# Optimization experiments

Measured on AMD Instinct MI355X. Metric: run time of the kernel, lower is better.

## Reference

```python
import jax, jax.numpy as jnp
import numpy as np

K = 5  # box-blur width along disparity axis

def _blur_disparity(x):
    # depthwise conv1d with ones(K)/K kernel, zero 'same' padding, along axis 1
    N, D, H, W = x.shape
    xp = jnp.pad(x, ((0, 0), (K // 2, K // 2), (0, 0), (0, 0)))
    acc = xp[:, 0:D]
    for s in range(1, K):
        acc = acc + xp[:, s:s + D]
    return acc / K

def _modal_mask(x):
    N, D, H, W = x.shape
    index = jnp.argmax(x, axis=1, keepdims=True)                 # [N,1,H,W] int
    d = jnp.arange(D, dtype=x.dtype).reshape(1, D, 1, 1)
    d2 = jnp.arange(D + 1, dtype=x.dtype).reshape(1, D + 1, 1, 1)
    ones = jnp.ones((N, 1, H, W), dtype=x.dtype)
    x_diff_r = jnp.diff(x, axis=1, prepend=ones, append=ones)    # [N,D+1,H,W]
    x_diff_l = jnp.diff(x, axis=1, prepend=ones)                 # [N,D,H,W]
    # right edge of dominant mode: first positive diff strictly right of peak
    ind_r = ((x_diff_r * (d2 > index)) > 0).astype(jnp.int32)
    index_r = jnp.argmax(ind_r, axis=1, keepdims=True) - 1
    # left edge: last negative diff at/left of peak
    ind_l = ((x_diff_l * (d <= index)) < 0).astype(jnp.int32)
    index_l = D - 1 - jnp.argmax(jnp.flip(ind_l, axis=1), axis=1, keepdims=True)
    mask1 = (d >= index_l) & (d <= index_r)
    r = jnp.minimum(index_r - index, index - index_l)
    mask2 = (d >= index - r) & (d <= index + r)
    valid = jnp.abs(2 * index - index_r - index_l) < 3           # near-symmetric mode
    return jnp.where(valid, mask1, mask2)                        # bool [N,D,H,W]

def setup_inputs() -> dict:
    key = jax.random.key(0)
    N, D, H, W = 2, 192, 256, 512
    x = jax.random.uniform(key, (N, D, H, W), dtype=jnp.float32)
    return {"x": x}

def reference(x) -> jnp.ndarray:
    N, D, H, W = x.shape
    disp = jnp.arange(D, dtype=x.dtype).reshape(1, D, 1, 1)
    x_blur = _blur_disparity(x)
    mask = _modal_mask(x_blur)
    y = x * mask                       # primary mode mass
    z = x - y
    x_blur2 = x_blur * (~mask)
    z = z * _modal_mask(x_blur2)       # secondary mode mass
    valid = (jnp.sum(y, axis=1) >= jnp.sum(z, axis=1)).astype(jnp.float32)[:, None]
    xm = valid * y + (1.0 - valid) * z
    xm = xm / jnp.sum(xm, axis=1, keepdims=True)
    out = jnp.sum(xm * disp, axis=1, keepdims=True)  # [N,1,H,W]
    return out
```

## Files before the change

kernel.cpp:

```cpp
#include <hip/hip_runtime.h>
#include <math.h>

namespace {
constexpr int D     = 192;
constexpr int HW    = 256 * 512;
constexpr int TOTAL = 2 * HW;

__device__ __forceinline__ float div5(float s) {
    const float c = 0.2f;
    float q = s * c;
    float r = __builtin_fmaf(-5.0f, q, s);
    return __builtin_fmaf(r, c, q);
}

__device__ __forceinline__ bool in_range(int d, int lo, unsigned width) {
    return (unsigned)(d - lo) <= width;
}

struct Machine {
    float bprev, maxv;
    int   index, last_fall, index_l, index_r;
    bool  r_found;

    __device__ __forceinline__ void init() {
        bprev = 1.0f;
        maxv  = -INFINITY;
        index = 0; last_fall = 0; index_l = 0;
        index_r = D - 1;
        r_found = false;
    }

    __device__ __forceinline__ void step(int d, float b) {
        float diff = b - bprev;
        bool fall  = diff < 0.0f;
        last_fall  = fall ? d : last_fall;
        bool am    = b > maxv;
        maxv       = am ? b : maxv;
        index      = am ? d : index;
        index_l    = am ? last_fall : index_l;
        bool rise  = (diff > 0.0f) & (!r_found) & (!am);
        index_r    = am ? (D - 1) : (rise ? (d - 1) : index_r);
        r_found    = am ? false : (r_found | rise);
        bprev      = b;
    }

    __device__ __forceinline__ void finish(int& lo, unsigned& wd) const {
        int r = min(index_r - index, index - index_l);
        int t = 2 * index - index_r - index_l;
        bool valid = (t > -3) && (t < 3);
        lo = valid ? index_l : (index - r);
        int hi = valid ? index_r : (index + r);
        wd = (unsigned)(hi - lo);
    }
};

template<int OFS>
__device__ __forceinline__ void loadc(const float* __restrict__ col, int c,
                                      float (&buf)[8]) {
    #pragma unroll
    for (int j = 0; j < 8; ++j)
        buf[j] = col[(size_t)(8 * c + OFS + j) * HW];
}
template<int OFS>
__device__ __forceinline__ void loadc_guard(const float* __restrict__ col, int c,
                                            float (&buf)[8]) {
    #pragma unroll
    for (int j = 0; j < 8; ++j) {
        int idx = 8 * c + OFS + j;
        buf[j] = (idx < D) ? col[(size_t)idx * HW] : 0.0f;
    }
}

template<int OFS, typename F>
__device__ __forceinline__ void stream24(const float* __restrict__ col, F&& f) {
    float A[8], B[8], C[8];
    loadc<OFS>(col, 0, A);
    loadc<OFS>(col, 1, B);
    loadc<OFS>(col, 2, C);
    int d = 0;
    auto comp = [&](float (&buf)[8]) {
        #pragma unroll
        for (int j = 0; j < 8; ++j) { f(d, buf[j]); ++d; }
    };
    for (int g = 0; g < 6; ++g) {
        comp(A); loadc<OFS>(col, 3 * g + 3, A);
        comp(B); loadc<OFS>(col, 3 * g + 4, B);
        comp(C); loadc<OFS>(col, 3 * g + 5, C);
    }
    comp(A); loadc<OFS>(col, 21, A);
    comp(B); loadc<OFS>(col, 22, B);
    comp(C);
    if (OFS == 2) loadc_guard<OFS>(col, 23, C);
    else          loadc<OFS>(col, 23, C);
    comp(A); comp(B); comp(C);
}
}

extern "C" __global__ void __launch_bounds__(256, 4)
dme_kernel(const float* __restrict__ x, float* __restrict__ out)
{
    const int n  = blockIdx.x >> 9;
    const int hw = ((blockIdx.x & 511) << 8) | threadIdx.x;
    const float* __restrict__ col = x + (size_t)n * (size_t)(D * HW) + hw;

    const float x0 = col[0];
    const float x1 = col[HW];

    Machine m1; m1.init();
    {
        float w0 = 0.f, w1 = 0.f, w2 = x0, w3 = x1;
        stream24<2>(col, [&](int d, float xv) {
            float s = w0 + w1; s += w2; s += w3; s += xv;
            m1.step(d, div5(s));
            w0 = w1; w1 = w2; w2 = w3; w3 = xv;
        });
    }
    int lo1; unsigned wd1; m1.finish(lo1, wd1);

    Machine m2; m2.init();
    float sum_y = 0.f, wsum_y = 0.f;
    {
        float w0 = 0.f, w1 = 0.f, w2 = x0, w3 = x1;
        float fd = 0.0f;
        stream24<2>(col, [&](int d, float xv) {
            float s = w0 + w1; s += w2; s += w3; s += xv;
            float b = div5(s);
            bool in1 = in_range(d, lo1, wd1);
            m2.step(d, in1 ? 0.0f : b);
            float xm = in1 ? w2 : 0.f;
            sum_y += xm;
            wsum_y = __builtin_fmaf(xm, fd, wsum_y);
            w0 = w1; w1 = w2; w2 = w3; w3 = xv; fd += 1.0f;
        });
    }
    int lo2; unsigned wd2; m2.finish(lo2, wd2);

    float sum_z = 0.f, wsum_z = 0.f;
    {
        const int dend = lo2 + (int)wd2;
        auto acc = [&](float xv, int dd) {
            bool  zz = !in_range(dd, lo1, wd1);
            float xm = zz ? xv : 0.0f;
            sum_z += xm;
            wsum_z = __builtin_fmaf(xm, (float)dd, wsum_z);
        };
        int dd = lo2;
        for (; dd + 3 <= dend; dd += 4) {
            float v0 = col[(size_t)(dd + 0) * HW];
            float v1 = col[(size_t)(dd + 1) * HW];
            float v2 = col[(size_t)(dd + 2) * HW];
            float v3 = col[(size_t)(dd + 3) * HW];
            acc(v0, dd + 0); acc(v1, dd + 1);
            acc(v2, dd + 2); acc(v3, dd + 3);
        }
        for (; dd <= dend; ++dd) acc(col[(size_t)dd * HW], dd);
    }

    bool  v = (sum_y >= sum_z);
    float S = v ? sum_y  : sum_z;
    float W = v ? wsum_y : wsum_z;
    out[hw + n * HW] = W / S;
}

extern "C" void kernel_launch(void* const* d_in, const int* in_sizes, int n_in,
                              void* d_out, int out_size, void* d_ws, size_t ws_size,
                              hipStream_t stream)
{
    const float* x   = (const float*)d_in[0];
    float*       out = (float*)d_out;
    dim3 block(256), grid(TOTAL / 256);
    hipLaunchKernelGGL(dme_kernel, grid, block, 0, stream, x, out);
}
```

Before: 315.8 us.

## Stream disparity rows through an LDS ring buffer with async global_load_lds

Replaces per-thread register-buffered global loads with a 32-row shared-memory ring. Each wavefront issues direct global-to-LDS 16-byte loads for one row slice, and a barrier plus vmcnt wait steps the pipeline every four rows. The aim is to keep more bytes in flight with fewer VGPRs and wider transactions. In exchange it adds a block-wide barrier per iteration and LDS traffic, and it relies on hand-written waitcnt accounting being correct.

```diff
diff --git a/kernel.cpp b/kernel.cpp
--- a/kernel.cpp
+++ b/kernel.cpp
@@ -5,6 +5,9 @@
 constexpr int D     = 192;
 constexpr int HW    = 256 * 512;
 constexpr int TOTAL = 2 * HW;
+constexpr unsigned ROWB = (unsigned)HW * 4u;
+
+typedef __attribute__((address_space(3))) char lds_char;
 
 __device__ __forceinline__ float div5(float s) {
     const float c = 0.2f;
@@ -53,66 +56,69 @@
         wd = (unsigned)(hi - lo);
     }
 };
-
-template<int OFS>
-__device__ __forceinline__ void loadc(const float* __restrict__ col, int c,
-                                      float (&buf)[8]) {
-    #pragma unroll
-    for (int j = 0; j < 8; ++j)
-        buf[j] = col[(size_t)(8 * c + OFS + j) * HW];
-}
-template<int OFS>
-__device__ __forceinline__ void loadc_guard(const float* __restrict__ col, int c,
-                                            float (&buf)[8]) {
-    #pragma unroll
-    for (int j = 0; j < 8; ++j) {
-        int idx = 8 * c + OFS + j;
-        buf[j] = (idx < D) ? col[(size_t)idx * HW] : 0.0f;
-    }
-}
-
-template<int OFS, typename F>
-__device__ __forceinline__ void stream24(const float* __restrict__ col, F&& f) {
-    float A[8], B[8], C[8];
-    loadc<OFS>(col, 0, A);
-    loadc<OFS>(col, 1, B);
-    loadc<OFS>(col, 2, C);
-    int d = 0;
-    auto comp = [&](float (&buf)[8]) {
-        #pragma unroll
-        for (int j = 0; j < 8; ++j) { f(d, buf[j]); ++d; }
-    };
-    for (int g = 0; g < 6; ++g) {
-        comp(A); loadc<OFS>(col, 3 * g + 3, A);
-        comp(B); loadc<OFS>(col, 3 * g + 4, B);
-        comp(C); loadc<OFS>(col, 3 * g + 5, C);
-    }
-    comp(A); loadc<OFS>(col, 21, A);
-    comp(B); loadc<OFS>(col, 22, B);
-    comp(C);
-    if (OFS == 2) loadc_guard<OFS>(col, 23, C);
-    else          loadc<OFS>(col, 23, C);
-    comp(A); comp(B); comp(C);
-}
 }
 
 extern "C" __global__ void __launch_bounds__(256, 4)
 dme_kernel(const float* __restrict__ x, float* __restrict__ out)
 {
-    const int n  = blockIdx.x >> 9;
-    const int hw = ((blockIdx.x & 511) << 8) | threadIdx.x;
-    const float* __restrict__ col = x + (size_t)n * (size_t)(D * HW) + hw;
+    __shared__ float ring[32 * 256];
+
+    const int tid  = threadIdx.x;
+    const int w    = tid >> 6;
+    const int lane = tid & 63;
+    const int n    = blockIdx.x >> 9;
+    const int hw0  = (blockIdx.x & 511) << 8;
+    const int hw   = hw0 | tid;
+    const float* __restrict__ xn = x + (size_t)n * (size_t)(D * HW);
+    const char* xb = (const char*)xn;
+    const unsigned hb4    = (unsigned)hw0 * 4u;
+    const unsigned lane16 = (unsigned)lane << 4;
+    const float* __restrict__ col = xn + hw;
 
     const float x0 = col[0];
     const float x1 = col[HW];
 
+    auto stage = [&](int e) {
+        const int dep = min(e + 2, D - 1);
+        __builtin_amdgcn_global_load_lds(
+            (__attribute__((address_space(1))) void*)
+                (xb + (unsigned)dep * ROWB + hb4 + lane16),
+            (__attribute__((address_space(3))) void*)
+                ((lds_char*)ring + (unsigned)((e & 31) << 10)),
+            16, 0, 0);
+    };
+
+    auto run_pass = [&](auto&& f) {
+        #pragma unroll
+        for (int i = 0; i < 7; ++i) stage(4 * i + w);
+        for (int r = 0; r < 48; ++r) {
+            asm volatile("s_waitcnt vmcnt(6)" ::: "memory");
+            __builtin_amdgcn_s_barrier();
+            asm volatile("" ::: "memory");
+            const int base = ((r & 7) << 10) + tid;
+            float v0 = ring[base];
+            float v1 = ring[base + 256];
+            float v2 = ring[base + 512];
+            float v3 = ring[base + 768];
+            const int d0 = 4 * r;
+            f(d0 + 0, v0);
+            f(d0 + 1, v1);
+            f(d0 + 2, (d0 + 2 >= D - 2) ? 0.0f : v2);
+            f(d0 + 3, (d0 + 3 >= D - 2) ? 0.0f : v3);
+            stage(d0 + 28 + w);
+        }
+        asm volatile("s_waitcnt vmcnt(0)" ::: "memory");
+        __builtin_amdgcn_s_barrier();
+        asm volatile("" ::: "memory");
+    };
+
     Machine m1; m1.init();
     {
-        float w0 = 0.f, w1 = 0.f, w2 = x0, w3 = x1;
-        stream24<2>(col, [&](int d, float xv) {
-            float s = w0 + w1; s += w2; s += w3; s += xv;
+        float a0 = 0.f, a1 = 0.f, a2 = x0, a3 = x1;
+        run_pass([&](int d, float xv) {
+            float s = a0 + a1; s += a2; s += a3; s += xv;
             m1.step(d, div5(s));
-            w0 = w1; w1 = w2; w2 = w3; w3 = xv;
+            a0 = a1; a1 = a2; a2 = a3; a3 = xv;
         });
     }
     int lo1; unsigned wd1; m1.finish(lo1, wd1);
@@ -120,17 +126,17 @@
     Machine m2; m2.init();
     float sum_y = 0.f, wsum_y = 0.f;
     {
-        float w0 = 0.f, w1 = 0.f, w2 = x0, w3 = x1;
+        float a0 = 0.f, a1 = 0.f, a2 = x0, a3 = x1;
         float fd = 0.0f;
-        stream24<2>(col, [&](int d, float xv) {
-            float s = w0 + w1; s += w2; s += w3; s += xv;
+        run_pass([&](int d, float xv) {
+            float s = a0 + a1; s += a2; s += a3; s += xv;
             float b = div5(s);
             bool in1 = in_range(d, lo1, wd1);
             m2.step(d, in1 ? 0.0f : b);
-            float xm = in1 ? w2 : 0.f;
+            float xm = in1 ? a2 : 0.f;
             sum_y += xm;
             wsum_y = __builtin_fmaf(xm, fd, wsum_y);
-            w0 = w1; w1 = w2; w2 = w3; w3 = xv; fd += 1.0f;
+            a0 = a1; a1 = a2; a2 = a3; a3 = xv; fd += 1.0f;
         });
     }
     int lo2; unsigned wd2; m2.finish(lo2, wd2);
```

Measured after the change: 321.7 us. About the same (+1.9%).
